# Performance work log

Measured on AMD Instinct MI355X. Metric: run time of the kernel, lower is better.

## Reference

```python
import jax, jax.numpy as jnp
import numpy as np

N_NODES = 50000
N_EDGES = 1600000
IN_CH = 128
HID = 128  # 2 * out_channels
NUM_GRAPHS = 64


def gcn_conv(x, row, col, ew, W, b, num_nodes):
    # PyG GCNConv: add self-loops (weight 1), symmetric degree norm, x @ W,
    # gather at source row, scale by norm, scatter-add at target col, add bias.
    loop = jnp.arange(num_nodes)
    r = jnp.concatenate([row, loop])
    c = jnp.concatenate([col, loop])
    w = jnp.concatenate([ew, jnp.ones((num_nodes,), ew.dtype)])
    deg = jax.ops.segment_sum(w, c, num_segments=num_nodes)
    dis = jnp.where(deg > 0, jax.lax.rsqrt(jnp.where(deg > 0, deg, 1.0)), 0.0)
    norm = dis[r] * w * dis[c]  # [E+N]
    xw = x @ W  # [N, HID]
    msg = xw[r] * norm[:, None]  # [E+N, HID] gather + scale
    out = jax.ops.segment_sum(msg, c, num_segments=num_nodes)
    return out + b


def setup_inputs() -> dict:
    key = jax.random.key(0)
    ks = jax.random.split(key, 8)
    x = jax.random.normal(ks[0], (N_NODES, IN_CH), dtype=jnp.float32)
    edge_index = jax.random.randint(ks[1], (2, N_EDGES), 0, N_NODES, dtype=jnp.int64)
    edge_weight = jax.random.uniform(ks[2], (N_EDGES,), dtype=jnp.float32)
    batch = jnp.sort(jax.random.randint(ks[3], (N_NODES,), 0, NUM_GRAPHS, dtype=jnp.int64))
    W1 = jax.random.normal(ks[4], (IN_CH, HID), dtype=jnp.float32) * 0.01
    b1 = jnp.zeros((HID,), jnp.float32)
    W2 = jax.random.normal(ks[5], (HID, HID), dtype=jnp.float32) * 0.01
    b2 = jnp.zeros((HID,), jnp.float32)
    return {"x": x, "edge_index": edge_index, "edge_weight": edge_weight,
            "batch": batch, "W1": W1, "b1": b1, "W2": W2, "b2": b2}


def reference(x, edge_index, edge_weight, batch, W1, b1, W2, b2):
    row, col = edge_index[0], edge_index[1]
    h = jax.nn.relu(gcn_conv(x, row, col, edge_weight, W1, b1, N_NODES))
    h = jax.nn.relu(gcn_conv(h, row, col, edge_weight, W2, b2, N_NODES))
    # global_mean_pool over batch segment ids
    sums = jax.ops.segment_sum(h, batch, num_segments=NUM_GRAPHS)
    cnts = jax.ops.segment_sum(jnp.ones((N_NODES,), h.dtype), batch, num_segments=NUM_GRAPHS)
    pooled = sums / jnp.maximum(cnts, 1.0)[:, None]
    return h, pooled
```

## Files before the change

kernel.cpp:

```cpp
#include <hip/hip_runtime.h>
#include <hip/hip_fp16.h>


#define CH 128
#define BSH 7
#define NBLK 1024
#define MAXNB 512
#define PCH 32
#define LDW 136

typedef __attribute__((ext_vector_type(8))) short bf16x8;
typedef __attribute__((ext_vector_type(4))) float f32x4;

static __device__ __forceinline__ unsigned short f2bf(float f) {
    unsigned u = __float_as_uint(f);
    unsigned r = (u + 0x7FFF + ((u >> 16) & 1)) >> 16;
    return (unsigned short)r;
}
static __device__ __forceinline__ float bflo(unsigned v) { return __uint_as_float(v << 16); }
static __device__ __forceinline__ float bfhi(unsigned v) { return __uint_as_float(v & 0xFFFF0000u); }
static __device__ __forceinline__ float f16u(unsigned bits15) {
    __half_raw hr; hr.x = (unsigned short)(bits15 & 0x7FFF);
    return __half2float(*reinterpret_cast<__half*>(&hr));
}
static __device__ __forceinline__ unsigned u16f(float f) {
    __half hh = __float2half(f);
    return (unsigned)(*reinterpret_cast<unsigned short*>(&hh)) & 0x7FFF;
}

__global__ __launch_bounds__(256) void k_sort1a(const int* __restrict__ col,
                                                int* __restrict__ H, int* __restrict__ cnt,
                                                int E, int NB, int chunk) {
    __shared__ int hist[MAXNB];
    int t = threadIdx.x, blk = blockIdx.x;
    if (blk == 0 && t == 0) *cnt = 0;
    for (int i = t; i < NB; i += 256) hist[i] = 0;
    __syncthreads();
    int s = blk * chunk, e1 = min(s + chunk, E);
    for (int e = s + t; e < e1; e += 256) atomicAdd(&hist[col[e] >> BSH], 1);
    __syncthreads();
    for (int i = t; i < NB; i += 256) H[(size_t)i * NBLK + blk] = hist[i];
}

__global__ __launch_bounds__(1024) void k_scan1(int* __restrict__ data,
                                                int* __restrict__ bsum,
                                                int* __restrict__ cnt, int n, int nb) {
    __shared__ int sd[1024];
    __shared__ int lastFlag;
    int t = threadIdx.x;
    int i = blockIdx.x * 1024 + t;
    int v = (i < n) ? data[i] : 0;
    sd[t] = v;
    __syncthreads();
    for (int off = 1; off < 1024; off <<= 1) {
        int u = (t >= off) ? sd[t - off] : 0;
        __syncthreads();
        sd[t] += u;
        __syncthreads();
    }
    if (i < n) data[i] = sd[t] - v;
    if (t == 1023) {
        bsum[blockIdx.x] = sd[1023];
        __threadfence();
        lastFlag = (atomicAdd(cnt, 1) == (int)gridDim.x - 1);
    }
    __syncthreads();
    if (lastFlag) {
        __threadfence();
        int v2 = (t < nb) ? bsum[t] : 0;
        sd[t] = v2;
        __syncthreads();
        for (int off = 1; off < 1024; off <<= 1) {
            int u = (t >= off) ? sd[t - off] : 0;
            __syncthreads();
            sd[t] += u;
            __syncthreads();
        }
        if (t < nb) bsum[t] = sd[t] - v2;
    }
}

__global__ __launch_bounds__(256) void k_sort1b(const int* __restrict__ row,
                                                const int* __restrict__ col,
                                                const float* __restrict__ ew,
                                                const int* __restrict__ Hs,
                                                const int* __restrict__ bsum,
                                                int2* __restrict__ pairs2,
                                                int E, int NB, int chunk) {
    __shared__ int cur[MAXNB];
    int t = threadIdx.x, blk = blockIdx.x;
    for (int i = t; i < NB; i += 256) cur[i] = Hs[(size_t)i * NBLK + blk] + bsum[i];
    __syncthreads();
    int s = blk * chunk, e1 = min(s + chunk, E);
    for (int e = s + t; e < e1; e += 256) {
        int c = col[e];
        int pos = atomicAdd(&cur[c >> BSH], 1);
        pairs2[pos] = make_int2(row[e] | ((c & 127) << 17), __float_as_int(ew[e]));
    }
}

__global__ __launch_bounds__(256) void k_sort2(const int* __restrict__ Hs,
                                               const int* __restrict__ bsum,
                                               const int2* __restrict__ pairs2,
                                               unsigned* __restrict__ epk,
                                               int* __restrict__ rowptr,
                                               float* __restrict__ dis,
                                               int E, int N, int NB) {
    __shared__ int hist[128];
    __shared__ int pref[128];
    __shared__ float wsum[128];
    int b = blockIdx.x, t = threadIdx.x;
    int n0 = b << BSH;
    int s = Hs[(size_t)b * NBLK] + bsum[b];
    int e1 = (b + 1 < NB) ? Hs[(size_t)(b + 1) * NBLK] + bsum[b + 1] : E;
    if (t < 128) { hist[t] = 0; wsum[t] = 0.f; }
    __syncthreads();
    for (int e = s + t; e < e1; e += 256)
        atomicAdd(&hist[(unsigned)pairs2[e].x >> 17], 1);
    __syncthreads();
    if (t < 128) pref[t] = hist[t];
    __syncthreads();
    for (int off = 1; off < 128; off <<= 1) {
        int v = 0;
        if (t < 128 && t >= off) v = pref[t - off];
        __syncthreads();
        if (t < 128) pref[t] += v;
        __syncthreads();
    }
    if (t < 128) {
        int excl = pref[t] - hist[t];
        int node = n0 + t;
        if (node < N) rowptr[node] = s + excl;
        hist[t] = s + excl;
    }
    if (b == NB - 1 && t == 0) rowptr[N] = E;
    __syncthreads();
    for (int e = s + t; e < e1; e += 256) {
        int2 pr = pairs2[e];
        int li = (unsigned)pr.x >> 17;
        float w = __int_as_float(pr.y);
        int pos = atomicAdd(&hist[li], 1);
        epk[pos] = (unsigned)(pr.x & 0x1FFFF) | (u16f(w) << 17);
        atomicAdd(&wsum[li], w);
    }
    __syncthreads();
    if (t < 128 && n0 + t < N) dis[n0 + t] = rsqrtf(1.0f + wsum[t]);
}

__global__ __launch_bounds__(64) void k_norm(const int* __restrict__ rowptr,
                                             unsigned* __restrict__ epk,
                                             const float* __restrict__ dis, int N) {
    int n = blockIdx.x;
    int lane = threadIdx.x;
    float dn = dis[n];
    int e0 = rowptr[n], e1 = rowptr[n + 1];
    for (int e = e0 + lane; e < e1; e += 64) {
        unsigned v = epk[e];
        unsigned src = v & 0x1FFFF;
        float nn = dn * f16u(v >> 17) * dis[src];
        epk[e] = src | (u16f(nn) << 17);
    }
}

__global__ __launch_bounds__(512) void k_gemm(const float* __restrict__ X,
                                              const float* __restrict__ W,
                                              unsigned short* __restrict__ Y, int N) {
    __shared__ unsigned short Wt[128 * LDW];
    int tid = threadIdx.x;
    for (int i = tid; i < 4096; i += 512) {
        float4 v = ((const float4*)W)[i];
        int k = i >> 5;
        int c = (i & 31) * 4;
        Wt[(c + 0) * LDW + k] = f2bf(v.x);
        Wt[(c + 1) * LDW + k] = f2bf(v.y);
        Wt[(c + 2) * LDW + k] = f2bf(v.z);
        Wt[(c + 3) * LDW + k] = f2bf(v.w);
    }
    __syncthreads();
    int w = tid >> 6, lane = tid & 63;
    int l15 = lane & 15, kg = lane >> 4;
    int r = blockIdx.x * 128 + w * 16 + l15;
    f32x4 acc[8];
#pragma unroll
    for (int ct = 0; ct < 8; ++ct) acc[ct] = (f32x4){0.f, 0.f, 0.f, 0.f};
#pragma unroll
    for (int kb = 0; kb < 128; kb += 32) {
        union { unsigned u[4]; bf16x8 v; } a;
        if (r < N) {
            const float4* xp = (const float4*)(X + (size_t)r * CH + kb + kg * 8);
            float4 x0 = xp[0], x1 = xp[1];
            a.u[0] = ((unsigned)f2bf(x0.y) << 16) | f2bf(x0.x);
            a.u[1] = ((unsigned)f2bf(x0.w) << 16) | f2bf(x0.z);
            a.u[2] = ((unsigned)f2bf(x1.y) << 16) | f2bf(x1.x);
            a.u[3] = ((unsigned)f2bf(x1.w) << 16) | f2bf(x1.z);
        } else {
            a.u[0] = a.u[1] = a.u[2] = a.u[3] = 0;
        }
#pragma unroll
        for (int ct = 0; ct < 8; ++ct) {
            bf16x8 b = *(const bf16x8*)&Wt[(ct * 16 + l15) * LDW + kb + kg * 8];
            acc[ct] = __builtin_amdgcn_mfma_f32_16x16x32_bf16(a.v, b, acc[ct], 0, 0, 0);
        }
    }
    int orow = blockIdx.x * 128 + w * 16 + kg * 4;
#pragma unroll
    for (int ct = 0; ct < 8; ++ct) {
#pragma unroll
        for (int j = 0; j < 4; ++j) {
            int rr = orow + j;
            if (rr < N) Y[(size_t)rr * CH + ct * 16 + l15] = f2bf(acc[ct][j]);
        }
    }
}

#define GATHER(p) XW[(size_t)((p) & 0x1FFFF) * 64 + lane]
#define ACC4(q, va, vb, vc, vd)                                           \
    {                                                                     \
        float na = f16u((q).x >> 17), nb = f16u((q).y >> 17);             \
        float nc = f16u((q).z >> 17), nd = f16u((q).w >> 17);             \
        ax += na * bflo(va) + nb * bflo(vb) + nc * bflo(vc) + nd * bflo(vd); \
        ay += na * bfhi(va) + nb * bfhi(vb) + nc * bfhi(vc) + nd * bfhi(vd); \
    }
__global__ __launch_bounds__(64) void k_agg(const unsigned int* __restrict__ XW,
                                            const float* __restrict__ dis,
                                            const int* __restrict__ rowptr,
                                            const unsigned* __restrict__ epk,
                                            const float* __restrict__ bias,
                                            float* __restrict__ OUT, int N) {
    int n = blockIdx.x;
    if (n >= N) return;
    int lane = threadIdx.x;
    float dn = dis[n];
    float sn = dn * dn;
    unsigned a = XW[(size_t)n * 64 + lane];
    float ax = bflo(a) * sn;
    float ay = bfhi(a) * sn;
    int e0 = rowptr[n], e1 = rowptr[n + 1];
    int e = e0;
    for (; e < e1 && (e & 3); ++e) {
        unsigned p = epk[e];
        unsigned v = GATHER(p);
        float nn = f16u(p >> 17);
        ax += nn * bflo(v);
        ay += nn * bfhi(v);
    }
    for (; e + 16 <= e1; e += 16) {
        uint4 q0 = *(const uint4*)&epk[e];
        uint4 q1 = *(const uint4*)&epk[e + 4];
        uint4 q2 = *(const uint4*)&epk[e + 8];
        uint4 q3 = *(const uint4*)&epk[e + 12];
        unsigned v0 = GATHER(q0.x), v1 = GATHER(q0.y), v2 = GATHER(q0.z), v3 = GATHER(q0.w);
        unsigned v4 = GATHER(q1.x), v5 = GATHER(q1.y), v6 = GATHER(q1.z), v7 = GATHER(q1.w);
        unsigned v8 = GATHER(q2.x), v9 = GATHER(q2.y), va = GATHER(q2.z), vb = GATHER(q2.w);
        unsigned vc = GATHER(q3.x), vd = GATHER(q3.y), ve = GATHER(q3.z), vf = GATHER(q3.w);
        ACC4(q0, v0, v1, v2, v3);
        ACC4(q1, v4, v5, v6, v7);
        ACC4(q2, v8, v9, va, vb);
        ACC4(q3, vc, vd, ve, vf);
    }
    for (; e + 4 <= e1; e += 4) {
        uint4 q = *(const uint4*)&epk[e];
        unsigned v0 = GATHER(q.x), v1 = GATHER(q.y), v2 = GATHER(q.z), v3 = GATHER(q.w);
        ACC4(q, v0, v1, v2, v3);
    }
    for (; e < e1; ++e) {
        unsigned p = epk[e];
        unsigned v = GATHER(p);
        float nn = f16u(p >> 17);
        ax += nn * bflo(v);
        ay += nn * bfhi(v);
    }
    float2 b = ((const float2*)bias)[lane];
    ax = fmaxf(ax + b.x, 0.f);
    ay = fmaxf(ay + b.y, 0.f);
    ((float2*)OUT)[(size_t)n * 64 + lane] = make_float2(ax, ay);
}

__device__ __forceinline__ int lowerb(const int* a, int n, int v) {
    int lo = 0, hi = n;
    while (lo < hi) {
        int m = (lo + hi) >> 1;
        if (a[m] < v) lo = m + 1; else hi = m;
    }
    return lo;
}

__global__ __launch_bounds__(128) void k_pool1(const float* __restrict__ H,
                                               const int* __restrict__ batch,
                                               float* __restrict__ partial, int N) {
    __shared__ int ss[2];
    int g = blockIdx.x / PCH;
    int k = blockIdx.x % PCH;
    if (threadIdx.x == 0) {
        ss[0] = lowerb(batch, N, g);
        ss[1] = lowerb(batch, N, g + 1);
    }
    __syncthreads();
    int s = ss[0], len = ss[1] - ss[0];
    int cs = s + (int)(((long long)len * k) / PCH);
    int ce = s + (int)(((long long)len * (k + 1)) / PCH);
    int ch = threadIdx.x;
    float a0 = 0.f, a1 = 0.f;
    int n = cs;
    for (; n + 2 <= ce; n += 2) {
        a0 += H[(size_t)(n + 0) * CH + ch];
        a1 += H[(size_t)(n + 1) * CH + ch];
    }
    for (; n < ce; ++n) a0 += H[(size_t)n * CH + ch];
    partial[(size_t)blockIdx.x * CH + ch] = a0 + a1;
}

__global__ __launch_bounds__(128) void k_pool2(const float* __restrict__ partial,
                                               const int* __restrict__ batch,
                                               float* __restrict__ P, int N) {
    __shared__ int ss[2];
    int g = blockIdx.x;
    if (threadIdx.x == 0) {
        ss[0] = lowerb(batch, N, g);
        ss[1] = lowerb(batch, N, g + 1);
    }
    __syncthreads();
    int ch = threadIdx.x;
    float a = 0.f;
#pragma unroll
    for (int k = 0; k < PCH; ++k) a += partial[(size_t)(g * PCH + k) * CH + ch];
    float c = (float)(ss[1] - ss[0]);
    P[(size_t)g * CH + ch] = a / fmaxf(c, 1.f);
}

extern "C" void kernel_launch(void* const* d_in, const int* in_sizes, int n_in,
                              void* d_out, int out_size, void* d_ws, size_t ws_size,
                              hipStream_t stream) {
    const float* x     = (const float*)d_in[0];
    const int*   ei    = (const int*)d_in[1];
    const float* ew    = (const float*)d_in[2];
    const int*   batch = (const int*)d_in[3];
    const float* W1    = (const float*)d_in[4];
    const float* b1    = (const float*)d_in[5];
    const float* W2    = (const float*)d_in[6];
    const float* b2    = (const float*)d_in[7];

    int N = in_sizes[0] / CH;
    int E = in_sizes[1] / 2;
    const int* row = ei;
    const int* col = ei + E;

    float* out    = (float*)d_out;
    float* h      = out;
    float* pooled = out + (size_t)N * CH;

    int NB    = (N + 127) >> BSH;
    int chunk = (E + NBLK - 1) / NBLK;
    int n2    = NB * NBLK;

    char* wsb = (char*)d_ws;
    size_t oN  = ((size_t)N * 4 + 255) & ~(size_t)255;
    size_t oN1 = ((size_t)(N + 1) * 4 + 255) & ~(size_t)255;
    size_t oH  = ((size_t)(n2 + 1) * 4 + 255) & ~(size_t)255;
    size_t oB  = 8192;
    size_t oE1 = ((size_t)E * 4 + 255) & ~(size_t)255;
    float* dis    = (float*)wsb;
    int*   rowptr = (int*)(wsb + oN);
    int*   H      = (int*)(wsb + oN + oN1);
    int*   bsum   = (int*)(wsb + oN + oN1 + oH);
    int*   cnt    = bsum + 1024;
    unsigned* epk = (unsigned*)(wsb + oN + oN1 + oH + oB);
    unsigned short* xw = (unsigned short*)(wsb + oN + oN1 + oH + oB + oE1);
    int2*  pairs2 = (int2*)xw;
    float* partial = (float*)H;

    int sb2 = (n2 + 1023) / 1024;

    k_sort1a<<<NBLK, 256, 0, stream>>>(col, H, cnt, E, NB, chunk);
    k_scan1<<<sb2, 1024, 0, stream>>>(H, bsum, cnt, n2, sb2);
    k_sort1b<<<NBLK, 256, 0, stream>>>(row, col, ew, H, bsum, pairs2, E, NB, chunk);
    k_sort2<<<NB, 256, 0, stream>>>(H, bsum, pairs2, epk, rowptr, dis, E, N, NB);
    k_norm<<<N, 64, 0, stream>>>(rowptr, epk, dis, N);

    int gb = (N + 127) / 128;
    k_gemm<<<gb, 512, 0, stream>>>(x, W1, xw, N);
    k_agg<<<N, 64, 0, stream>>>((const unsigned int*)xw, dis, rowptr, epk, b1, h, N);
    k_gemm<<<gb, 512, 0, stream>>>(h, W2, xw, N);
    k_agg<<<N, 64, 0, stream>>>((const unsigned int*)xw, dis, rowptr, epk, b2, h, N);
    k_pool1<<<64 * PCH, 128, 0, stream>>>(h, batch, partial, N);
    k_pool2<<<64, 128, 0, stream>>>(partial, batch, pooled, N);
}
```

Before: 233.7 us.

## Fold GCN normalization into GEMM/agg epilogues and keep layer-1 output in bf16

Removes the separate per-edge normalization pass by scaling GEMM output rows by the source degree factor and the aggregated sum by the target factor. Layer-1 activations are written as bf16 into a new workspace buffer and consumed by a new bf16-input GEMM, halving that intermediate's traffic. Aggregation now packs four nodes per 256-thread block. The risk is extra bf16 rounding of the hidden activations.

After: 232.4 us. Within noise of the previous version (-0.6%).

```diff
diff --git a/kernel.cpp b/kernel.cpp
--- a/kernel.cpp
+++ b/kernel.cpp
@@ -147,24 +147,10 @@
     if (t < 128 && n0 + t < N) dis[n0 + t] = rsqrtf(1.0f + wsum[t]);
 }
 
-__global__ __launch_bounds__(64) void k_norm(const int* __restrict__ rowptr,
-                                             unsigned* __restrict__ epk,
-                                             const float* __restrict__ dis, int N) {
-    int n = blockIdx.x;
-    int lane = threadIdx.x;
-    float dn = dis[n];
-    int e0 = rowptr[n], e1 = rowptr[n + 1];
-    for (int e = e0 + lane; e < e1; e += 64) {
-        unsigned v = epk[e];
-        unsigned src = v & 0x1FFFF;
-        float nn = dn * f16u(v >> 17) * dis[src];
-        epk[e] = src | (u16f(nn) << 17);
-    }
-}
-
-__global__ __launch_bounds__(512) void k_gemm(const float* __restrict__ X,
-                                              const float* __restrict__ W,
-                                              unsigned short* __restrict__ Y, int N) {
+__global__ __launch_bounds__(512) void k_gemm_f32(const float* __restrict__ X,
+                                                  const float* __restrict__ W,
+                                                  const float* __restrict__ dis,
+                                                  unsigned short* __restrict__ Y, int N) {
     __shared__ unsigned short Wt[128 * LDW];
     int tid = threadIdx.x;
     for (int i = tid; i < 4096; i += 512) {
@@ -203,38 +189,90 @@
         }
     }
     int orow = blockIdx.x * 128 + w * 16 + kg * 4;
+    float dv[4];
+#pragma unroll
+    for (int j = 0; j < 4; ++j) dv[j] = (orow + j < N) ? dis[orow + j] : 0.f;
 #pragma unroll
     for (int ct = 0; ct < 8; ++ct) {
 #pragma unroll
         for (int j = 0; j < 4; ++j) {
             int rr = orow + j;
-            if (rr < N) Y[(size_t)rr * CH + ct * 16 + l15] = f2bf(acc[ct][j]);
+            if (rr < N) Y[(size_t)rr * CH + ct * 16 + l15] = f2bf(acc[ct][j] * dv[j]);
+        }
+    }
+}
+
+__global__ __launch_bounds__(512) void k_gemm_bf16(const unsigned short* __restrict__ Xb,
+                                                   const float* __restrict__ W,
+                                                   const float* __restrict__ dis,
+                                                   unsigned short* __restrict__ Y, int N) {
+    __shared__ unsigned short Wt[128 * LDW];
+    int tid = threadIdx.x;
+    for (int i = tid; i < 4096; i += 512) {
+        float4 v = ((const float4*)W)[i];
+        int k = i >> 5;
+        int c = (i & 31) * 4;
+        Wt[(c + 0) * LDW + k] = f2bf(v.x);
+        Wt[(c + 1) * LDW + k] = f2bf(v.y);
+        Wt[(c + 2) * LDW + k] = f2bf(v.z);
+        Wt[(c + 3) * LDW + k] = f2bf(v.w);
+    }
+    __syncthreads();
+    int w = tid >> 6, lane = tid & 63;
+    int l15 = lane & 15, kg = lane >> 4;
+    int r = blockIdx.x * 128 + w * 16 + l15;
+    f32x4 acc[8];
+#pragma unroll
+    for (int ct = 0; ct < 8; ++ct) acc[ct] = (f32x4){0.f, 0.f, 0.f, 0.f};
+#pragma unroll
+    for (int kb = 0; kb < 128; kb += 32) {
+        bf16x8 a;
+        if (r < N) {
+            a = *(const bf16x8*)&Xb[(size_t)r * CH + kb + kg * 8];
+        } else {
+            a = (bf16x8){0, 0, 0, 0, 0, 0, 0, 0};
+        }
+#pragma unroll
+        for (int ct = 0; ct < 8; ++ct) {
+            bf16x8 b = *(const bf16x8*)&Wt[(ct * 16 + l15) * LDW + kb + kg * 8];
+            acc[ct] = __builtin_amdgcn_mfma_f32_16x16x32_bf16(a, b, acc[ct], 0, 0, 0);
+        }
+    }
+    int orow = blockIdx.x * 128 + w * 16 + kg * 4;
+    float dv[4];
+#pragma unroll
+    for (int j = 0; j < 4; ++j) dv[j] = (orow + j < N) ? dis[orow + j] : 0.f;
+#pragma unroll
+    for (int ct = 0; ct < 8; ++ct) {
+#pragma unroll
+        for (int j = 0; j < 4; ++j) {
+            int rr = orow + j;
+            if (rr < N) Y[(size_t)rr * CH + ct * 16 + l15] = f2bf(acc[ct][j] * dv[j]);
         }
     }
 }
 
 #define GATHER(p) XW[(size_t)((p) & 0x1FFFF) * 64 + lane]
-#define ACC4(q, va, vb, vc, vd)                                           \
-    {                                                                     \
-        float na = f16u((q).x >> 17), nb = f16u((q).y >> 17);             \
-        float nc = f16u((q).z >> 17), nd = f16u((q).w >> 17);             \
+#define ACC4(q, va, vb, vc, vd)                                              \
+    {                                                                        \
+        float na = f16u((q).x >> 17), nb = f16u((q).y >> 17);                \
+        float nc = f16u((q).z >> 17), nd = f16u((q).w >> 17);                \
         ax += na * bflo(va) + nb * bflo(vb) + nc * bflo(vc) + nd * bflo(vd); \
         ay += na * bfhi(va) + nb * bfhi(vb) + nc * bfhi(vc) + nd * bfhi(vd); \
     }
-__global__ __launch_bounds__(64) void k_agg(const unsigned int* __restrict__ XW,
-                                            const float* __restrict__ dis,
-                                            const int* __restrict__ rowptr,
-                                            const unsigned* __restrict__ epk,
-                                            const float* __restrict__ bias,
-                                            float* __restrict__ OUT, int N) {
-    int n = blockIdx.x;
+template <bool OUT_BF16>
+__global__ __launch_bounds__(256) void k_agg(const unsigned int* __restrict__ XW,
+                                             const float* __restrict__ dis,
+                                             const int* __restrict__ rowptr,
+                                             const unsigned* __restrict__ epk,
+                                             const float* __restrict__ bias,
+                                             void* __restrict__ OUT, int N) {
+    int n = blockIdx.x * 4 + (threadIdx.x >> 6);
     if (n >= N) return;
-    int lane = threadIdx.x;
-    float dn = dis[n];
-    float sn = dn * dn;
+    int lane = threadIdx.x & 63;
     unsigned a = XW[(size_t)n * 64 + lane];
-    float ax = bflo(a) * sn;
-    float ay = bfhi(a) * sn;
+    float ax = bflo(a);
+    float ay = bfhi(a);
     int e0 = rowptr[n], e1 = rowptr[n + 1];
     int e = e0;
     for (; e < e1 && (e & 3); ++e) {
@@ -270,10 +308,16 @@
         ax += nn * bflo(v);
         ay += nn * bfhi(v);
     }
+    float dn = dis[n];
     float2 b = ((const float2*)bias)[lane];
-    ax = fmaxf(ax + b.x, 0.f);
-    ay = fmaxf(ay + b.y, 0.f);
-    ((float2*)OUT)[(size_t)n * 64 + lane] = make_float2(ax, ay);
+    ax = fmaxf(fmaf(dn, ax, b.x), 0.f);
+    ay = fmaxf(fmaf(dn, ay, b.y), 0.f);
+    if (OUT_BF16) {
+        unsigned o = ((unsigned)f2bf(ay) << 16) | f2bf(ax);
+        ((unsigned*)OUT)[(size_t)n * 64 + lane] = o;
+    } else {
+        ((float2*)OUT)[(size_t)n * 64 + lane] = make_float2(ax, ay);
+    }
 }
 
 __device__ __forceinline__ int lowerb(const int* a, int n, int v) {
@@ -359,14 +403,18 @@
     size_t oH  = ((size_t)(n2 + 1) * 4 + 255) & ~(size_t)255;
     size_t oB  = 8192;
     size_t oE1 = ((size_t)E * 4 + 255) & ~(size_t)255;
+    size_t oE2 = ((size_t)E * 8 + 255) & ~(size_t)255;
     float* dis    = (float*)wsb;
     int*   rowptr = (int*)(wsb + oN);
     int*   H      = (int*)(wsb + oN + oN1);
     int*   bsum   = (int*)(wsb + oN + oN1 + oH);
     int*   cnt    = bsum + 1024;
     unsigned* epk = (unsigned*)(wsb + oN + oN1 + oH + oB);
-    unsigned short* xw = (unsigned short*)(wsb + oN + oN1 + oH + oB + oE1);
-    int2*  pairs2 = (int2*)xw;
+    char*  bufA   = wsb + oN + oN1 + oH + oB + oE1;
+    char*  bufB   = bufA + oE2;
+    int2*  pairs2 = (int2*)bufA;
+    unsigned short* xw = (unsigned short*)bufA;
+    unsigned short* h1 = (unsigned short*)bufB;
     float* partial = (float*)H;
 
     int sb2 = (n2 + 1023) / 1024;
@@ -375,13 +423,13 @@
     k_scan1<<<sb2, 1024, 0, stream>>>(H, bsum, cnt, n2, sb2);
     k_sort1b<<<NBLK, 256, 0, stream>>>(row, col, ew, H, bsum, pairs2, E, NB, chunk);
     k_sort2<<<NB, 256, 0, stream>>>(H, bsum, pairs2, epk, rowptr, dis, E, N, NB);
-    k_norm<<<N, 64, 0, stream>>>(rowptr, epk, dis, N);
 
     int gb = (N + 127) / 128;
-    k_gemm<<<gb, 512, 0, stream>>>(x, W1, xw, N);
-    k_agg<<<N, 64, 0, stream>>>((const unsigned int*)xw, dis, rowptr, epk, b1, h, N);
-    k_gemm<<<gb, 512, 0, stream>>>(h, W2, xw, N);
-    k_agg<<<N, 64, 0, stream>>>((const unsigned int*)xw, dis, rowptr, epk, b2, h, N);
+    int ab = (N + 3) / 4;
+    k_gemm_f32<<<gb, 512, 0, stream>>>(x, W1, dis, xw, N);
+    k_agg<true><<<ab, 256, 0, stream>>>((const unsigned int*)xw, dis, rowptr, epk, b1, h1, N);
+    k_gemm_bf16<<<gb, 512, 0, stream>>>(h1, W2, dis, xw, N);
+    k_agg<false><<<ab, 256, 0, stream>>>((const unsigned int*)xw, dis, rowptr, epk, b2, h, N);
     k_pool1<<<64 * PCH, 128, 0, stream>>>(h, batch, partial, N);
     k_pool2<<<64, 128, 0, stream>>>(partial, batch, pooled, N);
 }
```
